# Kernel tuning notes

Measured on AMD Instinct MI355X. Metric: run time of the kernel, lower is better.

The kernel has to match this reference:

```python
import jax, jax.numpy as jnp
import numpy as np

NEG_SLOPE = 0.2
BN_EPS = 1e-5
SM_EPS = 1e-16


def gatv2_conv(x, src, dst, num_nodes, Wl, bl, Wr, br, att, bias, concat):
    # x: [N, Fin]; att: [H, C]
    H, C = att.shape
    xl = (x @ Wl + bl).reshape(-1, H, C)  # source-side (x_j), lin_l
    xr = (x @ Wr + br).reshape(-1, H, C)  # target-side (x_i), lin_r
    e = jax.nn.leaky_relu(xl[src] + xr[dst], NEG_SLOPE)          # [E, H, C]
    logits = jnp.einsum('ehc,hc->eh', e, att)                    # [E, H]
    m = jax.ops.segment_max(logits, dst, num_segments=num_nodes)  # [N, H]
    expv = jnp.exp(logits - m[dst])
    denom = jax.ops.segment_sum(expv, dst, num_segments=num_nodes)
    alpha = expv / (denom[dst] + SM_EPS)                          # [E, H]
    msg = xl[src] * alpha[:, :, None]                             # [E, H, C]
    out = jax.ops.segment_sum(msg, dst, num_segments=num_nodes)   # [N, H, C]
    out = out.reshape(num_nodes, H * C) if concat else out.mean(axis=1)
    return out + bias


def batchnorm(x, gamma, beta):
    mean = x.mean(axis=0)
    var = x.var(axis=0)  # biased, as torch uses for normalization
    return gamma * (x - mean) * jax.lax.rsqrt(var + BN_EPS) + beta


def setup_inputs() -> dict:
    key = jax.random.key(0)
    ks = jax.random.split(key, 16)
    N, E = 50000, 800000
    Fin, Hid, Out, H = 128, 64, 64, 4
    s = 0.05
    inp = {
        'x': jax.random.normal(ks[0], (N, Fin), jnp.float32),
        'edge_index': jax.random.randint(ks[1], (2, E), 0, N, jnp.int64),
        # conv1 (heads=4, concat=False)
        'Wl1': jax.random.normal(ks[2], (Fin, H * Hid), jnp.float32) * s,
        'bl1': jnp.zeros((H * Hid,), jnp.float32),
        'Wr1': jax.random.normal(ks[3], (Fin, H * Hid), jnp.float32) * s,
        'br1': jnp.zeros((H * Hid,), jnp.float32),
        'att1': jax.random.normal(ks[4], (H, Hid), jnp.float32) * s,
        'bias1': jnp.zeros((Hid,), jnp.float32),
        'g1': jnp.ones((Hid,), jnp.float32),
        'beta1': jnp.zeros((Hid,), jnp.float32),
        # conv2 (heads=1, concat=True -> same as single head)
        'Wl2': jax.random.normal(ks[5], (Hid, Out), jnp.float32) * s,
        'bl2': jnp.zeros((Out,), jnp.float32),
        'Wr2': jax.random.normal(ks[6], (Hid, Out), jnp.float32) * s,
        'br2': jnp.zeros((Out,), jnp.float32),
        'att2': jax.random.normal(ks[7], (1, Out), jnp.float32) * s,
        'bias2': jnp.zeros((Out,), jnp.float32),
        'g2': jnp.ones((Out,), jnp.float32),
        'beta2': jnp.zeros((Out,), jnp.float32),
    }
    return inp


def reference(x, edge_index, Wl1, bl1, Wr1, br1, att1, bias1, g1, beta1,
              Wl2, bl2, Wr2, br2, att2, bias2, g2, beta2):
    N = x.shape[0]
    loops = jnp.arange(N, dtype=edge_index.dtype)  # PyG add_self_loops=True
    src = jnp.concatenate([edge_index[0], loops])
    dst = jnp.concatenate([edge_index[1], loops])
    h = gatv2_conv(x, src, dst, N, Wl1, bl1, Wr1, br1, att1, bias1, concat=False)
    h = jax.nn.relu(batchnorm(h, g1, beta1))  # dropout = identity (eval)
    h = gatv2_conv(h, src, dst, N, Wl2, bl2, Wr2, br2, att2, bias2, concat=True)
    h = jax.nn.relu(batchnorm(h, g2, beta2))
    return h
```

## Files before the change

### kernel.cpp

```cpp
#include <hip/hip_runtime.h>
#include <hip/hip_bf16.h>
#include <math.h>

#define TPB 256

typedef __attribute__((ext_vector_type(8))) _Float16 hfrag8;
typedef __attribute__((ext_vector_type(2))) _Float16 h2;
typedef __attribute__((ext_vector_type(4))) float f32x4;

union HU { unsigned int u; h2 h; };

static __device__ __forceinline__ h2 as_h2(unsigned int u) { HU c; c.u = u; return c.h; }
static __device__ __forceinline__ unsigned short f2h_bits(float f) {
  union { _Float16 h; unsigned short s; } c; c.h = (_Float16)f; return c.s;
}

#define DPP_ROR(v, C) __int_as_float(__builtin_amdgcn_update_dpp( \
    __float_as_int(v), __float_as_int(v), (C), 0xf, 0xf, false))
static __device__ __forceinline__ float red16(float p) {
  p += DPP_ROR(p, 0x121);
  p += DPP_ROR(p, 0x122);
  p += DPP_ROR(p, 0x124);
  p += DPP_ROR(p, 0x128);
  return p;
}

__global__ void k_prep_all(const int* __restrict__ ei, int E, int ET, int* __restrict__ deg,
                           const float* __restrict__ x,
                           const float* __restrict__ Wl1, const float* __restrict__ Wr1,
                           const float* __restrict__ Wl2, const float* __restrict__ Wr2,
                           unsigned short* __restrict__ xb,
                           unsigned short* __restrict__ wt1l, unsigned short* __restrict__ wt1r,
                           unsigned short* __restrict__ wt2l, unsigned short* __restrict__ wt2r,
                           int nx4) {
  int i = blockIdx.x * TPB + threadIdx.x;
  if (i < ET) {
    int dst = (i < E) ? ei[E + i] : (i - E);
    atomicAdd(&deg[dst], 1);
    return;
  }
  i -= ET;
  if (i < nx4) {
    float4 v = *(const float4*)(x + (size_t)i * 4);
    ushort4 o;
    o.x = f2h_bits(v.x); o.y = f2h_bits(v.y); o.z = f2h_bits(v.z); o.w = f2h_bits(v.w);
    *(ushort4*)(xb + (size_t)i * 4) = o;
    return;
  }
  i -= nx4;
  if (i < 32768) {
    int c = i >> 7, k = i & 127;
    wt1l[i] = f2h_bits(Wl1[(size_t)k * 256 + c]);
  } else if (i < 65536) {
    int j = i - 32768; int c = j >> 7, k = j & 127;
    wt1r[j] = f2h_bits(Wr1[(size_t)k * 256 + c]);
  } else if (i < 69632) {
    int j = i - 65536; int c = j >> 6, k = j & 63;
    wt2l[j] = f2h_bits(Wl2[(size_t)k * 64 + c]);
  } else if (i < 73728) {
    int j = i - 69632; int c = j >> 6, k = j & 63;
    wt2r[j] = f2h_bits(Wr2[(size_t)k * 64 + c]);
  }
}

__global__ void k_scan1(const int* __restrict__ deg, int N, int* __restrict__ bsum) {
  __shared__ int sm[TPB];
  int i = blockIdx.x * TPB + threadIdx.x;
  sm[threadIdx.x] = (i < N) ? ((deg[i] + 3) & ~3) : 0;
  __syncthreads();
  for (int d = TPB / 2; d > 0; d >>= 1) {
    if (threadIdx.x < d) sm[threadIdx.x] += sm[threadIdx.x + d];
    __syncthreads();
  }
  if (threadIdx.x == 0) bsum[blockIdx.x] = sm[0];
}

__global__ void k_scan3(const int* __restrict__ deg, const int* __restrict__ bsum,
                        int SB, int N, int* __restrict__ rowoff, int* __restrict__ cursor) {
  __shared__ int sm[TPB];
  int pv = (threadIdx.x < blockIdx.x) ? bsum[threadIdx.x] : 0;
  sm[threadIdx.x] = pv;
  __syncthreads();
  for (int dd = TPB / 2; dd > 0; dd >>= 1) {
    if (threadIdx.x < dd) sm[threadIdx.x] += sm[threadIdx.x + dd];
    __syncthreads();
  }
  int base = sm[0];
  __syncthreads();
  int i = blockIdx.x * TPB + threadIdx.x;
  int v = (i < N) ? ((deg[i] + 3) & ~3) : 0;
  sm[threadIdx.x] = v;
  __syncthreads();
  for (int dd = 1; dd < TPB; dd <<= 1) {
    int t = (threadIdx.x >= dd) ? sm[threadIdx.x - dd] : 0;
    __syncthreads();
    sm[threadIdx.x] += t;
    __syncthreads();
  }
  if (i < N) {
    int off = base + sm[threadIdx.x] - v;
    rowoff[i] = off;
    cursor[i] = off;
  }
}

__global__ void k_fill(const int* __restrict__ ei, int E, int ET,
                       int* __restrict__ cursor, int* __restrict__ csrc) {
  int e = blockIdx.x * blockDim.x + threadIdx.x;
  if (e >= ET) return;
  int src, dst;
  if (e < E) { src = ei[e]; dst = ei[E + e]; } else { src = dst = e - E; }
  int pos = atomicAdd(&cursor[dst], 1);
  csrc[pos] = src;
}

__global__ void k_gemm_mfma(const unsigned short* __restrict__ Ab,
                            const unsigned short* __restrict__ Wt0, const float* __restrict__ b0,
                            const unsigned short* __restrict__ Wt1, const float* __restrict__ b1,
                            unsigned short* __restrict__ out0, unsigned short* __restrict__ out1,
                            int M, int K, int Nc) {
  extern __shared__ short lds[];
  short* As = lds;
  short* Bls = lds + 64 * K;
  short* Brs = lds + 128 * K;
  const int r0 = blockIdx.x * 64, n0 = blockIdx.y * 64;
  const int tid = threadIdx.x;
  const int Kb = K * 2;
  const int cpr = K >> 3;
  const int chunks = 64 * cpr;
  for (int idx = tid; idx < chunks; idx += TPB) {
    int row = idx / cpr, k8 = (idx - row * cpr) * 8;
    int kb = (k8 * 2) ^ ((row & 7) << 4);
    int gr = r0 + row;
    uint4 av = make_uint4(0, 0, 0, 0);
    if (gr < M) av = *(const uint4*)(Ab + (size_t)gr * K + k8);
    *(uint4*)((char*)As + row * Kb + kb) = av;
    uint4 w0 = *(const uint4*)(Wt0 + (size_t)(n0 + row) * K + k8);
    *(uint4*)((char*)Bls + row * Kb + kb) = w0;
    uint4 w1 = *(const uint4*)(Wt1 + (size_t)(n0 + row) * K + k8);
    *(uint4*)((char*)Brs + row * Kb + kb) = w1;
  }
  __syncthreads();

  const int w = tid >> 6, lane = tid & 63;
  const int arow = w * 16 + (lane & 15);
  const int l16 = (lane >> 4) << 3;
  f32x4 accL[4], accR[4];
#pragma unroll
  for (int i = 0; i < 4; ++i) { accL[i] = (f32x4)0.f; accR[i] = (f32x4)0.f; }
  for (int k0 = 0; k0 < K; k0 += 32) {
    int kb = (k0 + l16) * 2;
    hfrag8 af = *(hfrag8*)((char*)As + arow * Kb + (kb ^ ((arow & 7) << 4)));
#pragma unroll
    for (int cf = 0; cf < 4; ++cf) {
      int col = cf * 16 + (lane & 15);
      int cb = col * Kb + (kb ^ ((col & 7) << 4));
      hfrag8 bl = *(hfrag8*)((char*)Bls + cb);
      accL[cf] = __builtin_amdgcn_mfma_f32_16x16x32_f16(af, bl, accL[cf], 0, 0, 0);
      hfrag8 br = *(hfrag8*)((char*)Brs + cb);
      accR[cf] = __builtin_amdgcn_mfma_f32_16x16x32_f16(af, br, accR[cf], 0, 0, 0);
    }
  }
  const int rbase = r0 + w * 16 + ((lane >> 4) << 2);
  const int cbase = n0 + (lane & 15);
#pragma unroll
  for (int cf = 0; cf < 4; ++cf) {
    int gcol = cbase + cf * 16;
    float bb0 = b0[gcol], bb1 = b1[gcol];
#pragma unroll
    for (int r = 0; r < 4; ++r) {
      int grow = rbase + r;
      if (grow < M) {
        out0[(size_t)grow * Nc + gcol] = f2h_bits(accL[cf][r] + bb0);
        out1[(size_t)grow * Nc + gcol] = f2h_bits(accR[cf][r] + bb1);
      }
    }
  }
}

__global__ __launch_bounds__(TPB) void k_gat1(
    const unsigned short* __restrict__ xl, const unsigned short* __restrict__ xr,
    const int* __restrict__ rowoff, const int* __restrict__ deg,
    const int* __restrict__ csrc,
    const float* __restrict__ att, const float* __restrict__ bias,
    float* __restrict__ out, int N) {
  int node = (blockIdx.x * TPB + threadIdx.x) >> 6;
  int lane = threadIdx.x & 63;
  if (node >= N) return;
  int l4 = lane * 4;
  float4 atv = *(const float4*)(att + l4);
  h2 at01, at23;
  at01.x = (_Float16)atv.x; at01.y = (_Float16)atv.y;
  at23.x = (_Float16)atv.z; at23.y = (_Float16)atv.w;
  float4 bb = *(const float4*)(bias + l4);
  uint2 rv = *(const uint2*)(xr + (node << 8) + l4);
  h2 xr01 = as_h2(rv.x), xr23 = as_h2(rv.y);
  const _Float16 c02 = (_Float16)0.2f;
  int beg = rowoff[node];
  int dg = deg[node];
  int endR = beg + dg;
  int endF = beg + (dg & ~3);
  float s = 0.f, a0 = 0.f, a1 = 0.f, a2 = 0.f, a3 = 0.f;
  int k = beg;
  for (; k < endF; k += 4) {
    int4 q = *(const int4*)(csrc + k);
    uint2 vv[4];
    vv[0] = *(const uint2*)(xl + (q.x << 8) + l4);
    vv[1] = *(const uint2*)(xl + (q.y << 8) + l4);
    vv[2] = *(const uint2*)(xl + (q.z << 8) + l4);
    vv[3] = *(const uint2*)(xl + (q.w << 8) + l4);
    float ps[4];
#pragma unroll
    for (int u = 0; u < 4; ++u) {
      h2 x01 = as_h2(vv[u].x), x23 = as_h2(vv[u].y);
      h2 t01 = x01 + xr01, t23 = x23 + xr23;
      h2 l01 = __builtin_elementwise_max(t01, t01 * c02);
      h2 l23 = __builtin_elementwise_max(t23, t23 * c02);
      ps[u] = __builtin_amdgcn_fdot2(l01, at01,
              __builtin_amdgcn_fdot2(l23, at23, 0.f, false), false);
    }
#pragma unroll
    for (int u = 0; u < 4; ++u) ps[u] = red16(ps[u]);
#pragma unroll
    for (int u = 0; u < 4; ++u) {
      float wv = __expf(ps[u]);
      h2 x01 = as_h2(vv[u].x), x23 = as_h2(vv[u].y);
      s += wv;
      a0 += wv * (float)x01.x; a1 += wv * (float)x01.y;
      a2 += wv * (float)x23.x; a3 += wv * (float)x23.y;
    }
  }
  if (k < endR) {
    int4 q = *(const int4*)(csrc + k);
    uint2 vv[4];
    vv[0] = *(const uint2*)(xl + (q.x << 8) + l4);
    vv[1] = *(const uint2*)(xl + (q.y << 8) + l4);
    vv[2] = *(const uint2*)(xl + (q.z << 8) + l4);
    vv[3] = *(const uint2*)(xl + (q.w << 8) + l4);
    float ps[4];
#pragma unroll
    for (int u = 0; u < 4; ++u) {
      h2 x01 = as_h2(vv[u].x), x23 = as_h2(vv[u].y);
      h2 t01 = x01 + xr01, t23 = x23 + xr23;
      h2 l01 = __builtin_elementwise_max(t01, t01 * c02);
      h2 l23 = __builtin_elementwise_max(t23, t23 * c02);
      ps[u] = __builtin_amdgcn_fdot2(l01, at01,
              __builtin_amdgcn_fdot2(l23, at23, 0.f, false), false);
    }
#pragma unroll
    for (int u = 0; u < 4; ++u) ps[u] = red16(ps[u]);
#pragma unroll
    for (int u = 0; u < 4; ++u) {
      float wv = (k + u < endR) ? __expf(ps[u]) : 0.f;
      h2 x01 = as_h2(vv[u].x), x23 = as_h2(vv[u].y);
      s += wv;
      a0 += wv * (float)x01.x; a1 += wv * (float)x01.y;
      a2 += wv * (float)x23.x; a3 += wv * (float)x23.y;
    }
  }
  float inv = 1.f / (s + 1e-16f);
  a0 *= inv; a1 *= inv; a2 *= inv; a3 *= inv;
  a0 += __shfl_xor(a0, 16); a0 += __shfl_xor(a0, 32);
  a1 += __shfl_xor(a1, 16); a1 += __shfl_xor(a1, 32);
  a2 += __shfl_xor(a2, 16); a2 += __shfl_xor(a2, 32);
  a3 += __shfl_xor(a3, 16); a3 += __shfl_xor(a3, 32);
  if (lane < 16) {
    float4 o;
    o.x = a0 * 0.25f + bb.x;
    o.y = a1 * 0.25f + bb.y;
    o.z = a2 * 0.25f + bb.z;
    o.w = a3 * 0.25f + bb.w;
    *(float4*)(out + (node << 6) + l4) = o;
  }
}

__global__ __launch_bounds__(TPB) void k_gat2(
    const unsigned short* __restrict__ xl, const unsigned short* __restrict__ xr,
    const int* __restrict__ rowoff, const int* __restrict__ deg,
    const int* __restrict__ csrc,
    const float* __restrict__ att, const float* __restrict__ bias,
    float* __restrict__ out, int N) {
  int node = (blockIdx.x * TPB + threadIdx.x) >> 6;
  int lane = threadIdx.x & 63;
  if (node >= N) return;
  int grp = lane >> 4, c4 = (lane & 15) * 4;
  float4 atv = *(const float4*)(att + c4);
  h2 at01, at23;
  at01.x = (_Float16)atv.x; at01.y = (_Float16)atv.y;
  at23.x = (_Float16)atv.z; at23.y = (_Float16)atv.w;
  float4 bb = *(const float4*)(bias + c4);
  uint2 rv = *(const uint2*)(xr + (node << 6) + c4);
  h2 xr01 = as_h2(rv.x), xr23 = as_h2(rv.y);
  const _Float16 c02 = (_Float16)0.2f;
  int beg = rowoff[node];
  int dg = deg[node];
  int endR = beg + dg;
  int quads = (dg + 3) >> 2;
  float s = 0.f, a0 = 0.f, a1 = 0.f, a2 = 0.f, a3 = 0.f;
  for (int it = 0; it < quads; ++it) {
    int kk = beg + it * 4 + grp;
    int src = csrc[kk];
    bool ok = kk < endR;
    uint2 v = *(const uint2*)(xl + (src << 6) + c4);
    h2 x01 = as_h2(v.x), x23 = as_h2(v.y);
    h2 t01 = x01 + xr01, t23 = x23 + xr23;
    h2 l01 = __builtin_elementwise_max(t01, t01 * c02);
    h2 l23 = __builtin_elementwise_max(t23, t23 * c02);
    float p = __builtin_amdgcn_fdot2(l01, at01,
              __builtin_amdgcn_fdot2(l23, at23, 0.f, false), false);
    p = red16(p);
    float wv = ok ? __expf(p) : 0.f;
    s += wv;
    a0 += wv * (float)x01.x; a1 += wv * (float)x01.y;
    a2 += wv * (float)x23.x; a3 += wv * (float)x23.y;
  }
  s += __shfl_xor(s, 16); s += __shfl_xor(s, 32);
  a0 += __shfl_xor(a0, 16); a0 += __shfl_xor(a0, 32);
  a1 += __shfl_xor(a1, 16); a1 += __shfl_xor(a1, 32);
  a2 += __shfl_xor(a2, 16); a2 += __shfl_xor(a2, 32);
  a3 += __shfl_xor(a3, 16); a3 += __shfl_xor(a3, 32);
  if (lane < 16) {
    float inv = 1.f / (s + 1e-16f);
    float4 o;
    o.x = a0 * inv + bb.x;
    o.y = a1 * inv + bb.y;
    o.z = a2 * inv + bb.z;
    o.w = a3 * inv + bb.w;
    *(float4*)(out + (node << 6) + c4) = o;
  }
}

__global__ void k_bnstat(const float* __restrict__ in, int N, float* __restrict__ part) {
  __shared__ float sm[TPB], sq[TPB];
  int col = threadIdx.x & 63;
  int rq = threadIdx.x >> 6;
  float s = 0.f, q = 0.f;
  for (int r = blockIdx.x * 4 + rq; r < N; r += gridDim.x * 4) {
    float v = in[(size_t)r * 64 + col];
    s += v; q += v * v;
  }
  sm[threadIdx.x] = s; sq[threadIdx.x] = q;
  __syncthreads();
  if (threadIdx.x < 64) {
    s = sm[threadIdx.x] + sm[threadIdx.x + 64] + sm[threadIdx.x + 128] + sm[threadIdx.x + 192];
    q = sq[threadIdx.x] + sq[threadIdx.x + 64] + sq[threadIdx.x + 128] + sq[threadIdx.x + 192];
    part[(size_t)blockIdx.x * 128 + threadIdx.x] = s;
    part[(size_t)blockIdx.x * 128 + 64 + threadIdx.x] = q;
  }
}

__global__ void k_bnfin(const float* __restrict__ part, int B, int N,
                        const float* __restrict__ g, const float* __restrict__ beta,
                        float* __restrict__ ab) {
  int c = threadIdx.x;
  float s = 0.f, q = 0.f;
  for (int b = 0; b < B; ++b) {
    s += part[(size_t)b * 128 + c];
    q += part[(size_t)b * 128 + 64 + c];
  }
  float mean = s / (float)N;
  float var = q / (float)N - mean * mean;
  float a = g[c] * rsqrtf(var + 1e-5f);
  ab[c] = a;
  ab[64 + c] = beta[c] - mean * a;
}

__global__ void k_prep2(const float* __restrict__ in, const float* __restrict__ ab,
                        unsigned short* __restrict__ o, int n4) {
  int i = blockIdx.x * blockDim.x + threadIdx.x;
  if (i >= n4) return;
  float4 v = *(const float4*)(in + (size_t)i * 4);
  int c0 = (i & 15) * 4;
  ushort4 u;
  u.x = f2h_bits(fmaxf(v.x * ab[c0 + 0] + ab[64 + c0 + 0], 0.f));
  u.y = f2h_bits(fmaxf(v.y * ab[c0 + 1] + ab[64 + c0 + 1], 0.f));
  u.z = f2h_bits(fmaxf(v.z * ab[c0 + 2] + ab[64 + c0 + 2], 0.f));
  u.w = f2h_bits(fmaxf(v.w * ab[c0 + 3] + ab[64 + c0 + 3], 0.f));
  *(ushort4*)(o + (size_t)i * 4) = u;
}

__global__ void k_bnapply(const float* __restrict__ in, const float* __restrict__ ab,
                          float* __restrict__ out, int total4) {
  int idx = blockIdx.x * blockDim.x + threadIdx.x;
  if (idx >= total4) return;
  float4 v = *(const float4*)(in + (size_t)idx * 4);
  int c0 = (idx & 15) * 4;
  v.x = fmaxf(v.x * ab[c0 + 0] + ab[64 + c0 + 0], 0.f);
  v.y = fmaxf(v.y * ab[c0 + 1] + ab[64 + c0 + 1], 0.f);
  v.z = fmaxf(v.z * ab[c0 + 2] + ab[64 + c0 + 2], 0.f);
  v.w = fmaxf(v.w * ab[c0 + 3] + ab[64 + c0 + 3], 0.f);
  *(float4*)(out + (size_t)idx * 4) = v;
}

extern "C" void kernel_launch(void* const* d_in, const int* in_sizes, int n_in,
                              void* d_out, int out_size, void* d_ws, size_t ws_size,
                              hipStream_t stream) {
  const float* x     = (const float*)d_in[0];
  const int*   ei    = (const int*)d_in[1];
  const float* Wl1   = (const float*)d_in[2];
  const float* bl1   = (const float*)d_in[3];
  const float* Wr1   = (const float*)d_in[4];
  const float* br1   = (const float*)d_in[5];
  const float* att1  = (const float*)d_in[6];
  const float* bias1 = (const float*)d_in[7];
  const float* g1    = (const float*)d_in[8];
  const float* be1   = (const float*)d_in[9];
  const float* Wl2   = (const float*)d_in[10];
  const float* bl2   = (const float*)d_in[11];
  const float* Wr2   = (const float*)d_in[12];
  const float* br2   = (const float*)d_in[13];
  const float* att2  = (const float*)d_in[14];
  const float* bias2 = (const float*)d_in[15];
  const float* g2    = (const float*)d_in[16];
  const float* be2   = (const float*)d_in[17];
  float* out = (float*)d_out;

  const int N  = in_sizes[0] / 128;
  const int E  = in_sizes[1] / 2;
  const int ET = E + N;
  const int ETP = ET + 4 * ((N + 255) & ~255);
  const int SB = (N + TPB - 1) / TPB;

  char* p = (char*)d_ws;
  auto take = [&](size_t b) { char* q = p; p += (b + 255) & ~(size_t)255; return q; };

  unsigned short* xl1 = (unsigned short*)take((size_t)N * 256 * 2);
  unsigned short* xr1 = (unsigned short*)take((size_t)N * 256 * 2);
  unsigned short* xl2 = (unsigned short*)take((size_t)N * 64 * 2);
  unsigned short* xr2 = (unsigned short*)take((size_t)N * 64 * 2);
  float* out1 = (float*)take((size_t)N * 64 * 4);
  unsigned short* xb = (unsigned short*)take((size_t)N * 128 * 2);
  unsigned short* wt1l = (unsigned short*)take(256 * 128 * 2);
  unsigned short* wt1r = (unsigned short*)take(256 * 128 * 2);
  unsigned short* wt2l = (unsigned short*)take(64 * 64 * 2);
  unsigned short* wt2r = (unsigned short*)take(64 * 64 * 2);
  int* deg    = (int*)take((size_t)N * 4);
  int* csrc   = (int*)take((size_t)ETP * 4 + 16);
  size_t zero_bytes = (char*)(csrc + ETP) + 16 - (char*)deg;
  int* rowoff = (int*)take((size_t)(N + 1) * 4);
  int* cursor = (int*)take((size_t)N * 4);
  int* bsum   = (int*)take((size_t)SB * 4);
  float* part = (float*)take((size_t)256 * 128 * 4);
  float* ab1  = (float*)take(128 * 4);
  float* ab2  = (float*)take(128 * 4);
  (void)ws_size; (void)n_in; (void)out_size;

  unsigned short* A2 = xb;

  int egrid = (ET + TPB - 1) / TPB;
  int nx4 = N * 32;
  int ptot = ET + nx4 + 73728;
  int ngrid = (N + 3) / 4;
  int mtile = (N + 63) / 64;
  int total4 = N * 16;

  hipMemsetAsync(deg, 0, zero_bytes, stream);
  k_prep_all<<<(ptot + TPB - 1) / TPB, TPB, 0, stream>>>(
      ei, E, ET, deg, x, Wl1, Wr1, Wl2, Wr2, xb, wt1l, wt1r, wt2l, wt2r, nx4);
  k_scan1<<<SB, TPB, 0, stream>>>(deg, N, bsum);
  k_scan3<<<SB, TPB, 0, stream>>>(deg, bsum, SB, N, rowoff, cursor);
  k_fill<<<egrid, TPB, 0, stream>>>(ei, E, ET, cursor, csrc);

  k_gemm_mfma<<<dim3(mtile, 4), TPB, 3 * 64 * 128 * 2, stream>>>(
      xb, wt1l, bl1, wt1r, br1, xl1, xr1, N, 128, 256);
  k_gat1<<<ngrid, TPB, 0, stream>>>(xl1, xr1, rowoff, deg, csrc, att1, bias1, out1, N);
  k_bnstat<<<256, TPB, 0, stream>>>(out1, N, part);
  k_bnfin<<<1, 64, 0, stream>>>(part, 256, N, g1, be1, ab1);

  k_prep2<<<(total4 + TPB - 1) / TPB, TPB, 0, stream>>>(out1, ab1, A2, total4);
  k_gemm_mfma<<<dim3(mtile, 1), TPB, 3 * 64 * 64 * 2, stream>>>(
      A2, wt2l, bl2, wt2r, br2, xl2, xr2, N, 64, 64);
  k_gat2<<<ngrid, TPB, 0, stream>>>(xl2, xr2, rowoff, deg, csrc, att2, bias2, out, N);
  k_bnstat<<<256, TPB, 0, stream>>>(out, N, part);
  k_bnfin<<<1, 64, 0, stream>>>(part, 256, N, g2, be2, ab2);
  k_bnapply<<<(total4 + TPB - 1) / TPB, TPB, 0, stream>>>(out, ab2, out, total4);
}
```

Baseline: 414.0 us.

## Fuse fp16 conversion and BN-affine into GEMM loads, merge scan and BN finalize kernels

The GEMM now reads fp32 activations directly and converts them to fp16 while staging into LDS. For layer 2 it also applies the batchnorm affine and ReLU there, which removes the separate x-conversion and prep2 passes and their intermediate buffers. The two-pass block scan becomes one kernel in which each block redundantly sums all preceding degrees. BN statistics and finalize are merged using a last-block atomic counter. Together these cut kernel launches and global traffic, at the cost of redundant prefix reads in the scan and a serial tail in the last BN block. In the first GEMM, each A tile is now re-read in fp32 and reconverted by all four column blocks.

```diff
diff --git a/kernel.cpp b/kernel.cpp
--- a/kernel.cpp
+++ b/kernel.cpp
@@ -25,29 +25,22 @@
   return p;
 }
 
-__global__ void k_prep_all(const int* __restrict__ ei, int E, int ET, int* __restrict__ deg,
-                           const float* __restrict__ x,
-                           const float* __restrict__ Wl1, const float* __restrict__ Wr1,
-                           const float* __restrict__ Wl2, const float* __restrict__ Wr2,
-                           unsigned short* __restrict__ xb,
-                           unsigned short* __restrict__ wt1l, unsigned short* __restrict__ wt1r,
-                           unsigned short* __restrict__ wt2l, unsigned short* __restrict__ wt2r,
-                           int nx4) {
-  int i = blockIdx.x * TPB + threadIdx.x;
-  if (i < ET) {
-    int dst = (i < E) ? ei[E + i] : (i - E);
-    atomicAdd(&deg[dst], 1);
+__global__ void k_deg_wprep(const int* __restrict__ ei, int E, int ET, int* __restrict__ deg,
+                            const float* __restrict__ Wl1, const float* __restrict__ Wr1,
+                            const float* __restrict__ Wl2, const float* __restrict__ Wr2,
+                            unsigned short* __restrict__ wt1l, unsigned short* __restrict__ wt1r,
+                            unsigned short* __restrict__ wt2l, unsigned short* __restrict__ wt2r,
+                            int egrid) {
+  int b = blockIdx.x;
+  if (b < egrid) {
+    int e = b * TPB + threadIdx.x;
+    if (e < ET) {
+      int dst = (e < E) ? ei[E + e] : (e - E);
+      atomicAdd(&deg[dst], 1);
+    }
     return;
   }
-  i -= ET;
-  if (i < nx4) {
-    float4 v = *(const float4*)(x + (size_t)i * 4);
-    ushort4 o;
-    o.x = f2h_bits(v.x); o.y = f2h_bits(v.y); o.z = f2h_bits(v.z); o.w = f2h_bits(v.w);
-    *(ushort4*)(xb + (size_t)i * 4) = o;
-    return;
-  }
-  i -= nx4;
+  int i = (b - egrid) * TPB + threadIdx.x;
   if (i < 32768) {
     int c = i >> 7, k = i & 127;
     wt1l[i] = f2h_bits(Wl1[(size_t)k * 256 + c]);
@@ -63,42 +56,33 @@
   }
 }
 
-__global__ void k_scan1(const int* __restrict__ deg, int N, int* __restrict__ bsum) {
+__global__ void k_scanf(const int* __restrict__ deg, int N,
+                        int* __restrict__ rowoff, int* __restrict__ cursor) {
   __shared__ int sm[TPB];
-  int i = blockIdx.x * TPB + threadIdx.x;
-  sm[threadIdx.x] = (i < N) ? ((deg[i] + 3) & ~3) : 0;
+  int t = threadIdx.x;
+  int pref = blockIdx.x * TPB;
+  int acc = 0;
+  for (int j = t; j < pref; j += TPB) acc += (deg[j] + 3) & ~3;
+  sm[t] = acc;
   __syncthreads();
   for (int d = TPB / 2; d > 0; d >>= 1) {
-    if (threadIdx.x < d) sm[threadIdx.x] += sm[threadIdx.x + d];
+    if (t < d) sm[t] += sm[t + d];
     __syncthreads();
   }
-  if (threadIdx.x == 0) bsum[blockIdx.x] = sm[0];
-}
-
-__global__ void k_scan3(const int* __restrict__ deg, const int* __restrict__ bsum,
-                        int SB, int N, int* __restrict__ rowoff, int* __restrict__ cursor) {
-  __shared__ int sm[TPB];
-  int pv = (threadIdx.x < blockIdx.x) ? bsum[threadIdx.x] : 0;
-  sm[threadIdx.x] = pv;
-  __syncthreads();
-  for (int dd = TPB / 2; dd > 0; dd >>= 1) {
-    if (threadIdx.x < dd) sm[threadIdx.x] += sm[threadIdx.x + dd];
+  int base = sm[0];
+  __syncthreads();
+  int i = pref + t;
+  int v = (i < N) ? ((deg[i] + 3) & ~3) : 0;
+  sm[t] = v;
+  __syncthreads();
+  for (int d = 1; d < TPB; d <<= 1) {
+    int tmp = (t >= d) ? sm[t - d] : 0;
     __syncthreads();
-  }
-  int base = sm[0];
-  __syncthreads();
-  int i = blockIdx.x * TPB + threadIdx.x;
-  int v = (i < N) ? ((deg[i] + 3) & ~3) : 0;
-  sm[threadIdx.x] = v;
-  __syncthreads();
-  for (int dd = 1; dd < TPB; dd <<= 1) {
-    int t = (threadIdx.x >= dd) ? sm[threadIdx.x - dd] : 0;
+    sm[t] += tmp;
     __syncthreads();
-    sm[threadIdx.x] += t;
-    __syncthreads();
   }
   if (i < N) {
-    int off = base + sm[threadIdx.x] - v;
+    int off = base + sm[t] - v;
     rowoff[i] = off;
     cursor[i] = off;
   }
@@ -114,7 +98,7 @@
   csrc[pos] = src;
 }
 
-__global__ void k_gemm_mfma(const unsigned short* __restrict__ Ab,
+__global__ void k_gemm_mfma(const float* __restrict__ A, const float* __restrict__ affine,
                             const unsigned short* __restrict__ Wt0, const float* __restrict__ b0,
                             const unsigned short* __restrict__ Wt1, const float* __restrict__ b1,
                             unsigned short* __restrict__ out0, unsigned short* __restrict__ out1,
@@ -126,19 +110,33 @@
   const int r0 = blockIdx.x * 64, n0 = blockIdx.y * 64;
   const int tid = threadIdx.x;
   const int Kb = K * 2;
+
+  const int fpr = K >> 2;
+  for (int idx = tid; idx < 64 * fpr; idx += TPB) {
+    int row = idx / fpr, c4 = idx - row * fpr;
+    int gr = r0 + row;
+    float4 v = make_float4(0.f, 0.f, 0.f, 0.f);
+    if (gr < M) v = *(const float4*)(A + (size_t)gr * K + c4 * 4);
+    if (affine) {
+      int c = c4 * 4;
+      v.x = fmaxf(v.x * affine[c + 0] + affine[64 + c + 0], 0.f);
+      v.y = fmaxf(v.y * affine[c + 1] + affine[64 + c + 1], 0.f);
+      v.z = fmaxf(v.z * affine[c + 2] + affine[64 + c + 2], 0.f);
+      v.w = fmaxf(v.w * affine[c + 3] + affine[64 + c + 3], 0.f);
+    }
+    ushort4 pk;
+    pk.x = f2h_bits(v.x); pk.y = f2h_bits(v.y); pk.z = f2h_bits(v.z); pk.w = f2h_bits(v.w);
+    int kb = (c4 * 8) ^ ((row & 7) << 4);
+    *(ushort4*)((char*)As + row * Kb + kb) = pk;
+  }
   const int cpr = K >> 3;
-  const int chunks = 64 * cpr;
-  for (int idx = tid; idx < chunks; idx += TPB) {
-    int row = idx / cpr, k8 = (idx - row * cpr) * 8;
-    int kb = (k8 * 2) ^ ((row & 7) << 4);
-    int gr = r0 + row;
-    uint4 av = make_uint4(0, 0, 0, 0);
-    if (gr < M) av = *(const uint4*)(Ab + (size_t)gr * K + k8);
-    *(uint4*)((char*)As + row * Kb + kb) = av;
-    uint4 w0 = *(const uint4*)(Wt0 + (size_t)(n0 + row) * K + k8);
-    *(uint4*)((char*)Bls + row * Kb + kb) = w0;
-    uint4 w1 = *(const uint4*)(Wt1 + (size_t)(n0 + row) * K + k8);
-    *(uint4*)((char*)Brs + row * Kb + kb) = w1;
+  for (int idx = tid; idx < 64 * cpr; idx += TPB) {
+    int c = idx / cpr, k8 = (idx - c * cpr) * 8;
+    int kb = (k8 * 2) ^ ((c & 7) << 4);
+    uint4 w0 = *(const uint4*)(Wt0 + (size_t)(n0 + c) * K + k8);
+    *(uint4*)((char*)Bls + c * Kb + kb) = w0;
+    uint4 w1 = *(const uint4*)(Wt1 + (size_t)(n0 + c) * K + k8);
+    *(uint4*)((char*)Brs + c * Kb + kb) = w1;
   }
   __syncthreads();
 
@@ -330,8 +328,11 @@
   }
 }
 
-__global__ void k_bnstat(const float* __restrict__ in, int N, float* __restrict__ part) {
+__global__ void k_bnstatfin(const float* __restrict__ in, int N, float* __restrict__ part,
+                            int* __restrict__ counter, const float* __restrict__ g,
+                            const float* __restrict__ beta, float* __restrict__ ab) {
   __shared__ float sm[TPB], sq[TPB];
+  __shared__ int lastsm;
   int col = threadIdx.x & 63;
   int rq = threadIdx.x >> 6;
   float s = 0.f, q = 0.f;
@@ -347,36 +348,26 @@
     part[(size_t)blockIdx.x * 128 + threadIdx.x] = s;
     part[(size_t)blockIdx.x * 128 + 64 + threadIdx.x] = q;
   }
-}
-
-__global__ void k_bnfin(const float* __restrict__ part, int B, int N,
-                        const float* __restrict__ g, const float* __restrict__ beta,
-                        float* __restrict__ ab) {
-  int c = threadIdx.x;
-  float s = 0.f, q = 0.f;
-  for (int b = 0; b < B; ++b) {
-    s += part[(size_t)b * 128 + c];
-    q += part[(size_t)b * 128 + 64 + c];
-  }
-  float mean = s / (float)N;
-  float var = q / (float)N - mean * mean;
-  float a = g[c] * rsqrtf(var + 1e-5f);
-  ab[c] = a;
-  ab[64 + c] = beta[c] - mean * a;
-}
-
-__global__ void k_prep2(const float* __restrict__ in, const float* __restrict__ ab,
-                        unsigned short* __restrict__ o, int n4) {
-  int i = blockIdx.x * blockDim.x + threadIdx.x;
-  if (i >= n4) return;
-  float4 v = *(const float4*)(in + (size_t)i * 4);
-  int c0 = (i & 15) * 4;
-  ushort4 u;
-  u.x = f2h_bits(fmaxf(v.x * ab[c0 + 0] + ab[64 + c0 + 0], 0.f));
-  u.y = f2h_bits(fmaxf(v.y * ab[c0 + 1] + ab[64 + c0 + 1], 0.f));
-  u.z = f2h_bits(fmaxf(v.z * ab[c0 + 2] + ab[64 + c0 + 2], 0.f));
-  u.w = f2h_bits(fmaxf(v.w * ab[c0 + 3] + ab[64 + c0 + 3], 0.f));
-  *(ushort4*)(o + (size_t)i * 4) = u;
+  __threadfence();
+  __syncthreads();
+  if (threadIdx.x == 0) lastsm = atomicAdd(counter, 1);
+  __syncthreads();
+  if (lastsm == gridDim.x - 1) {
+    __threadfence();
+    if (threadIdx.x < 64) {
+      int c = threadIdx.x;
+      float ts = 0.f, tq = 0.f;
+      for (int b = 0; b < gridDim.x; ++b) {
+        ts += part[(size_t)b * 128 + c];
+        tq += part[(size_t)b * 128 + 64 + c];
+      }
+      float mean = ts / (float)N;
+      float var = tq / (float)N - mean * mean;
+      float a = g[c] * rsqrtf(var + 1e-5f);
+      ab[c] = a;
+      ab[64 + c] = beta[c] - mean * a;
+    }
+  }
 }
 
 __global__ void k_bnapply(const float* __restrict__ in, const float* __restrict__ ab,
@@ -429,49 +420,41 @@
   unsigned short* xl2 = (unsigned short*)take((size_t)N * 64 * 2);
   unsigned short* xr2 = (unsigned short*)take((size_t)N * 64 * 2);
   float* out1 = (float*)take((size_t)N * 64 * 4);
-  unsigned short* xb = (unsigned short*)take((size_t)N * 128 * 2);
   unsigned short* wt1l = (unsigned short*)take(256 * 128 * 2);
   unsigned short* wt1r = (unsigned short*)take(256 * 128 * 2);
   unsigned short* wt2l = (unsigned short*)take(64 * 64 * 2);
   unsigned short* wt2r = (unsigned short*)take(64 * 64 * 2);
   int* deg    = (int*)take((size_t)N * 4);
+  int* ctr    = (int*)take(512);
   int* csrc   = (int*)take((size_t)ETP * 4 + 16);
   size_t zero_bytes = (char*)(csrc + ETP) + 16 - (char*)deg;
   int* rowoff = (int*)take((size_t)(N + 1) * 4);
   int* cursor = (int*)take((size_t)N * 4);
-  int* bsum   = (int*)take((size_t)SB * 4);
   float* part = (float*)take((size_t)256 * 128 * 4);
   float* ab1  = (float*)take(128 * 4);
   float* ab2  = (float*)take(128 * 4);
   (void)ws_size; (void)n_in; (void)out_size;
 
-  unsigned short* A2 = xb;
-
   int egrid = (ET + TPB - 1) / TPB;
-  int nx4 = N * 32;
-  int ptot = ET + nx4 + 73728;
+  int wgrid = (73728 + TPB - 1) / TPB;
   int ngrid = (N + 3) / 4;
   int mtile = (N + 63) / 64;
   int total4 = N * 16;
 
   hipMemsetAsync(deg, 0, zero_bytes, stream);
-  k_prep_all<<<(ptot + TPB - 1) / TPB, TPB, 0, stream>>>(
-      ei, E, ET, deg, x, Wl1, Wr1, Wl2, Wr2, xb, wt1l, wt1r, wt2l, wt2r, nx4);
-  k_scan1<<<SB, TPB, 0, stream>>>(deg, N, bsum);
-  k_scan3<<<SB, TPB, 0, stream>>>(deg, bsum, SB, N, rowoff, cursor);
+  k_deg_wprep<<<egrid + wgrid, TPB, 0, stream>>>(ei, E, ET, deg, Wl1, Wr1, Wl2, Wr2,
+                                                 wt1l, wt1r, wt2l, wt2r, egrid);
+  k_scanf<<<SB, TPB, 0, stream>>>(deg, N, rowoff, cursor);
   k_fill<<<egrid, TPB, 0, stream>>>(ei, E, ET, cursor, csrc);
 
   k_gemm_mfma<<<dim3(mtile, 4), TPB, 3 * 64 * 128 * 2, stream>>>(
-      xb, wt1l, bl1, wt1r, br1, xl1, xr1, N, 128, 256);
+      x, nullptr, wt1l, bl1, wt1r, br1, xl1, xr1, N, 128, 256);
   k_gat1<<<ngrid, TPB, 0, stream>>>(xl1, xr1, rowoff, deg, csrc, att1, bias1, out1, N);
-  k_bnstat<<<256, TPB, 0, stream>>>(out1, N, part);
-  k_bnfin<<<1, 64, 0, stream>>>(part, 256, N, g1, be1, ab1);
-
-  k_prep2<<<(total4 + TPB - 1) / TPB, TPB, 0, stream>>>(out1, ab1, A2, total4);
+  k_bnstatfin<<<256, TPB, 0, stream>>>(out1, N, part, ctr, g1, be1, ab1);
+
   k_gemm_mfma<<<dim3(mtile, 1), TPB, 3 * 64 * 64 * 2, stream>>>(
-      A2, wt2l, bl2, wt2r, br2, xl2, xr2, N, 64, 64);
+      out1, ab1, wt2l, bl2, wt2r, br2, xl2, xr2, N, 64, 64);
   k_gat2<<<ngrid, TPB, 0, stream>>>(xl2, xr2, rowoff, deg, csrc, att2, bias2, out, N);
-  k_bnstat<<<256, TPB, 0, stream>>>(out, N, part);
-  k_bnfin<<<1, 64, 0, stream>>>(part, 256, N, g2, be2, ab2);
+  k_bnstatfin<<<256, TPB, 0, stream>>>(out, N, part, ctr + 64, g2, be2, ab2);
   k_bnapply<<<(total4 + TPB - 1) / TPB, TPB, 0, stream>>>(out, ab2, out, total4);
 }
```

Result: slower. 476.9 us (+15.2%).
